# Kernel optimization log

Hardware: AMD Instinct MI355X
Metric: run time of the kernel (lower is better)

The kernel has to match this reference:

```python
import math
import jax, jax.numpy as jnp
import numpy as np

LAMDA = 0.5
ALPHA = 0.1
N_NODES = 100000
N_EDGES = 1600000
NFEAT = 512
NHID = 128
NCLASS = 40
NLAYER = 4


def setup_inputs() -> dict:
    key = jax.random.key(0)
    ks = jax.random.split(key, 9)
    x = jax.random.normal(ks[0], (N_NODES, NFEAT), dtype=jnp.float32)
    rows = jnp.sort(jax.random.randint(ks[1], (N_EDGES,), 0, N_NODES, dtype=jnp.int32))
    cols = jax.random.randint(ks[2], (N_EDGES,), 0, N_NODES, dtype=jnp.int32)
    # positive edge weights (stand-in for symmetric-normalized adjacency values)
    vals = jax.random.uniform(ks[3], (N_EDGES,), dtype=jnp.float32) * 0.1
    stdv_hid = 1.0 / math.sqrt(NHID)
    fc1_w = jax.random.normal(ks[4], (NFEAT, NHID), dtype=jnp.float32) * 0.02
    fc1_b = jnp.zeros((NHID,), dtype=jnp.float32)
    conv_w = jax.random.uniform(ks[5], (NLAYER, NHID, NHID), dtype=jnp.float32,
                                minval=-stdv_hid, maxval=stdv_hid)
    fc2_w = jax.random.normal(ks[6], (NHID, NCLASS), dtype=jnp.float32) * 0.02
    fc2_b = jnp.zeros((NCLASS,), dtype=jnp.float32)
    return {"x": x, "rows": rows, "cols": cols, "vals": vals,
            "fc1_w": fc1_w, "fc1_b": fc1_b, "conv_w": conv_w,
            "fc2_w": fc2_w, "fc2_b": fc2_b}


def reference(x, rows, cols, vals, fc1_w, fc1_b, conv_w, fc2_w, fc2_b):
    n = x.shape[0]
    # input projection + relu (dropout is identity in eval mode)
    h = jax.nn.relu(x @ fc1_w + fc1_b)  # [N, nhid]
    h0 = h
    for i in range(conv_w.shape[0]):
        theta = math.log(LAMDA / (i + 1) + 1.0)
        # sparse spmm: hi = A @ h  via gather + segment-sum scatter
        hi = jax.ops.segment_sum(vals[:, None] * h[cols], rows, num_segments=n)
        support = (1.0 - ALPHA) * hi + ALPHA * h0  # initial-residual mix
        h = jax.nn.relu(theta * (support @ conv_w[i]) + (1.0 - theta) * support)
    logits = h @ fc2_w + fc2_b  # [N, nclass]
    return (jax.nn.log_softmax(logits, axis=1), h, jnp.concatenate([h, logits], axis=1))
```

## Files before the change

### kernel.cpp

```cpp
#include <hip/hip_runtime.h>
#include <math.h>

#define N_NODES 100000
#define NFEAT 512
#define NHID 128
#define NCLASS 40

typedef unsigned int uint;
typedef unsigned short ushort;
typedef unsigned char uchar;
typedef short bf16x8 __attribute__((ext_vector_type(8)));
typedef float f32x4 __attribute__((ext_vector_type(4)));
typedef float f32x2 __attribute__((ext_vector_type(2)));

__device__ inline ushort bf16s(float a) {
    uint u = __float_as_uint(a);
    return (ushort)((u + 0x7fffu + ((u >> 16) & 1u)) >> 16);
}
__device__ inline uint bf16pack(float a, float b) {
    return (uint)bf16s(a) | ((uint)bf16s(b) << 16);
}
__device__ inline float bf16tof(ushort u) { return __uint_as_float(((uint)u) << 16); }
__device__ inline float bflo(uint u) { return __uint_as_float(u << 16); }
__device__ inline float bfhi(uint u) { return __uint_as_float(u & 0xffff0000u); }

__device__ inline uchar fp8byte(float v) {
    uint pk = __builtin_amdgcn_cvt_pk_fp8_f32(v, 0.f, 0u, false);
    return (uchar)(pk & 0xffu);
}

__global__ void prep_weights(const float* __restrict__ fc1_w, const float* __restrict__ conv_w,
                             ushort* __restrict__ wT1, ushort* __restrict__ wTc) {
    int idx = blockIdx.x * 256 + threadIdx.x;
    {   int n = idx >> 9, k = idx & 511;
        wT1[idx] = bf16s(fc1_w[k * NHID + n]); }
    {   int L = idx >> 14, rem = idx & 16383;
        int n = rem >> 7, k = rem & 127;
        wTc[idx] = bf16s(conv_w[L * 16384 + k * NHID + n]); }
}

__global__ void rowptr_kernel(const int* __restrict__ rows, int* __restrict__ rowptr, int nE) {
    int i = blockIdx.x * blockDim.x + threadIdx.x;
    if (i > N_NODES) return;
    int lo = 0, hi = nE;
    while (lo < hi) { int mid = (lo + hi) >> 1; if (rows[mid] < i) lo = mid + 1; else hi = mid; }
    rowptr[i] = lo;
}

__global__ void __launch_bounds__(256) fc1_mfma(const float* __restrict__ x,
                                                const uint* __restrict__ wT1,
                                                const float* __restrict__ bias,
                                                ushort* __restrict__ h0b,
                                                uchar* __restrict__ hf8) {
    __shared__ ushort As[32][72];
    __shared__ ushort Bs[128][72];
    const int tid = threadIdx.x;
    const int lane = tid & 63;
    const int wave = tid >> 6;
    const int wr = wave >> 1, wc = wave & 1;
    const int r0 = blockIdx.x * 32;

    f32x4 acc[4] = {};

    for (int ks = 0; ks < NFEAT; ks += 64) {
        {   int row = tid >> 3, kq = tid & 7;
            const float* xp = x + (size_t)(r0 + row) * NFEAT + ks + kq * 8;
            float4 v0 = *reinterpret_cast<const float4*>(xp);
            float4 v1 = *reinterpret_cast<const float4*>(xp + 4);
            uint4 pk;
            pk.x = bf16pack(v0.x, v0.y); pk.y = bf16pack(v0.z, v0.w);
            pk.z = bf16pack(v1.x, v1.y); pk.w = bf16pack(v1.z, v1.w);
            *reinterpret_cast<uint4*>(&As[row][kq * 8]) = pk;
        }
        #pragma unroll
        for (int p = 0; p < 4; ++p) {
            int idx = tid + p * 256;
            int n = idx >> 3, q = idx & 7;
            uint4 w4 = *reinterpret_cast<const uint4*>(wT1 + n * 256 + (ks >> 1) + q * 4);
            *reinterpret_cast<uint4*>(&Bs[n][q * 8]) = w4;
        }
        __syncthreads();
        #pragma unroll
        for (int ks2 = 0; ks2 < 64; ks2 += 32) {
            bf16x8 a = *reinterpret_cast<const bf16x8*>(&As[wr * 16 + (lane & 15)][ks2 + (lane >> 4) * 8]);
            #pragma unroll
            for (int j = 0; j < 4; ++j) {
                bf16x8 b = *reinterpret_cast<const bf16x8*>(&Bs[wc * 64 + j * 16 + (lane & 15)][ks2 + (lane >> 4) * 8]);
                acc[j] = __builtin_amdgcn_mfma_f32_16x16x32_bf16(a, b, acc[j], 0, 0, 0);
            }
        }
        __syncthreads();
    }

    const int cb = wc * 64 + (lane & 15);
    const int rb = r0 + wr * 16 + ((lane >> 4) << 2);
    #pragma unroll
    for (int j = 0; j < 4; ++j) {
        int col = cb + j * 16;
        float bj = bias[col];
        #pragma unroll
        for (int i = 0; i < 4; ++i) {
            float v = fmaxf(acc[j][i] + bj, 0.f);
            h0b[(size_t)(rb + i) * NHID + col] = bf16s(v);
            hf8[(size_t)(rb + i) * NHID + col] = fp8byte(v);
        }
    }
}

__global__ void __launch_bounds__(256) spmm_kernel(
        const uint2* __restrict__ h8,
        const uint4* __restrict__ h0b4,
        const int* __restrict__ rowptr,
        const int* __restrict__ cols,
        const float* __restrict__ vals,
        uint4* __restrict__ sb4) {
    const int node = blockIdx.x * 4 + (threadIdx.x >> 6);
    const int lane = threadIdx.x & 63;
    const int q = lane >> 4;
    const int l = lane & 15;

    const int e0 = rowptr[node], e1 = rowptr[node + 1];

    f32x2 a0 = {0.f, 0.f}, a1 = {0.f, 0.f}, a2 = {0.f, 0.f}, a3 = {0.f, 0.f};
    #pragma unroll 4
    for (int e = e0 + q; e < e1; e += 4) {
        int   c = cols[e];
        float v = vals[e];
        uint2 hv = h8[(size_t)c * 16 + l];
        f32x2 p0 = __builtin_amdgcn_cvt_pk_f32_fp8(hv.x, false);
        f32x2 p1 = __builtin_amdgcn_cvt_pk_f32_fp8(hv.x, true);
        f32x2 p2 = __builtin_amdgcn_cvt_pk_f32_fp8(hv.y, false);
        f32x2 p3 = __builtin_amdgcn_cvt_pk_f32_fp8(hv.y, true);
        f32x2 vv = {v, v};
        a0 += vv * p0;
        a1 += vv * p1;
        a2 += vv * p2;
        a3 += vv * p3;
    }

    #pragma unroll
    for (int d = 16; d <= 32; d <<= 1) {
        a0.x += __shfl_xor(a0.x, d); a0.y += __shfl_xor(a0.y, d);
        a1.x += __shfl_xor(a1.x, d); a1.y += __shfl_xor(a1.y, d);
        a2.x += __shfl_xor(a2.x, d); a2.y += __shfl_xor(a2.y, d);
        a3.x += __shfl_xor(a3.x, d); a3.y += __shfl_xor(a3.y, d);
    }

    if (q == 0) {
        uint4 h0v = h0b4[(size_t)node * 16 + l];
        uint4 o;
        o.x = bf16pack(0.9f * a0.x + 0.1f * bflo(h0v.x), 0.9f * a0.y + 0.1f * bfhi(h0v.x));
        o.y = bf16pack(0.9f * a1.x + 0.1f * bflo(h0v.y), 0.9f * a1.y + 0.1f * bfhi(h0v.y));
        o.z = bf16pack(0.9f * a2.x + 0.1f * bflo(h0v.z), 0.9f * a2.y + 0.1f * bfhi(h0v.z));
        o.w = bf16pack(0.9f * a3.x + 0.1f * bflo(h0v.w), 0.9f * a3.y + 0.1f * bfhi(h0v.w));
        sb4[(size_t)node * 16 + l] = o;
    }
}

__global__ void __launch_bounds__(256) layer_mfma(const uint* __restrict__ sb,
                                                  const uint* __restrict__ wTc,
                                                  float theta,
                                                  uchar* __restrict__ hf8,
                                                  float* __restrict__ fout) {
    __shared__ ushort As[64][136];
    __shared__ ushort Bs[128][136];
    const int tid = threadIdx.x;
    const int lane = tid & 63;
    const int wave = tid >> 6;
    const int wr = wave >> 1, wc = wave & 1;
    const int r0 = blockIdx.x * 64;

    #pragma unroll
    for (int p = 0; p < 4; ++p) {
        int idx = tid + p * 256;
        int row = idx >> 4, kq = idx & 15;
        uint4 v = *reinterpret_cast<const uint4*>(sb + (size_t)(r0 + row) * 64 + kq * 4);
        *reinterpret_cast<uint4*>(&As[row][kq * 8]) = v;
    }
    #pragma unroll
    for (int p = 0; p < 8; ++p) {
        int idx = tid + p * 256;
        int n = idx >> 4, kq = idx & 15;
        uint4 v = *reinterpret_cast<const uint4*>(wTc + n * 64 + kq * 4);
        *reinterpret_cast<uint4*>(&Bs[n][kq * 8]) = v;
    }
    __syncthreads();

    f32x4 acc[2][4] = {};
    #pragma unroll
    for (int ks = 0; ks < NHID; ks += 32) {
        #pragma unroll
        for (int mr = 0; mr < 2; ++mr) {
            bf16x8 a = *reinterpret_cast<const bf16x8*>(&As[wr * 32 + mr * 16 + (lane & 15)][ks + (lane >> 4) * 8]);
            #pragma unroll
            for (int j = 0; j < 4; ++j) {
                bf16x8 b = *reinterpret_cast<const bf16x8*>(&Bs[wc * 64 + j * 16 + (lane & 15)][ks + (lane >> 4) * 8]);
                acc[mr][j] = __builtin_amdgcn_mfma_f32_16x16x32_bf16(a, b, acc[mr][j], 0, 0, 0);
            }
        }
    }

    const float om = 1.f - theta;
    #pragma unroll
    for (int mr = 0; mr < 2; ++mr) {
        const int rloc = wr * 32 + mr * 16 + ((lane >> 4) << 2);
        #pragma unroll
        for (int j = 0; j < 4; ++j) {
            int col = wc * 64 + j * 16 + (lane & 15);
            #pragma unroll
            for (int i = 0; i < 4; ++i) {
                int gr = r0 + rloc + i;
                if (gr < N_NODES) {
                    float s = bf16tof(As[rloc + i][col]);
                    float v = fmaxf(fmaf(theta, acc[mr][j][i], om * s), 0.f);
                    if (fout) fout[(size_t)gr * NHID + col] = v;
                    else      hf8[(size_t)gr * NHID + col] = fp8byte(v);
                }
            }
        }
    }
}

__global__ void final_kernel(const float* __restrict__ h, const float* __restrict__ w,
                             const float* __restrict__ b, float* __restrict__ out0,
                             float* __restrict__ out2) {
    __shared__ float hs[4][128];
    const int s = threadIdx.x >> 6;
    const int lane = threadIdx.x & 63;
    const int node = blockIdx.x * 4 + s;

    float h_lo = h[node * NHID + lane];
    float h_hi = h[node * NHID + 64 + lane];
    hs[s][lane] = h_lo;
    hs[s][64 + lane] = h_hi;
    __syncthreads();

    float logit = 0.f;
    if (lane < NCLASS) {
        logit = b[lane];
        #pragma unroll 8
        for (int k = 0; k < NHID; ++k)
            logit = fmaf(hs[s][k], w[k * NCLASS + lane], logit);
    }

    float mv = (lane < NCLASS) ? logit : -1e30f;
    #pragma unroll
    for (int m = 32; m; m >>= 1) mv = fmaxf(mv, __shfl_xor(mv, m));
    float ev = (lane < NCLASS) ? __expf(logit - mv) : 0.f;
    float sum = ev;
    #pragma unroll
    for (int m = 32; m; m >>= 1) sum += __shfl_xor(sum, m);
    float lse = mv + __logf(sum);

    if (lane < NCLASS) {
        out0[node * NCLASS + lane] = logit - lse;
        out2[node * 168 + 128 + lane] = logit;
    }
    out2[node * 168 + lane] = h_lo;
    out2[node * 168 + 64 + lane] = h_hi;
}

extern "C" void kernel_launch(void* const* d_in, const int* in_sizes, int n_in,
                              void* d_out, int out_size, void* d_ws, size_t ws_size,
                              hipStream_t stream) {
    const float* x      = (const float*)d_in[0];
    const int*   rows   = (const int*)  d_in[1];
    const int*   cols   = (const int*)  d_in[2];
    const float* vals   = (const float*)d_in[3];
    const float* fc1_w  = (const float*)d_in[4];
    const float* fc1_b  = (const float*)d_in[5];
    const float* conv_w = (const float*)d_in[6];
    const float* fc2_w  = (const float*)d_in[7];
    const float* fc2_b  = (const float*)d_in[8];
    float* out = (float*)d_out;

    const int nE = in_sizes[1];
    const size_t NH = (size_t)N_NODES * NHID;
    const size_t PAD = 64 * NHID;

    char* p = (char*)d_ws;
    int*    rowptr = (int*)p;          p += 400128;
    ushort* h0b    = (ushort*)p;       p += NH * 2;
    ushort* sb     = (ushort*)p;       p += (NH + PAD) * 2;
    uchar*  hf8    = (uchar*)p;        p += NH;
    ushort* wT1    = (ushort*)p;       p += 65536 * 2;
    ushort* wTc    = (ushort*)p;       p += 65536 * 2;

    float* out0 = out;
    float* out1 = out + (size_t)N_NODES * NCLASS;
    float* out2 = out1 + NH;

    prep_weights<<<256, 256, 0, stream>>>(fc1_w, conv_w, wT1, wTc);
    rowptr_kernel<<<(N_NODES + 1 + 255) / 256, 256, 0, stream>>>(rows, rowptr, nE);
    fc1_mfma<<<N_NODES / 32, 256, 0, stream>>>(x, (const uint*)wT1, fc1_b, h0b, hf8);

    for (int i = 0; i < 4; ++i) {
        float theta = logf(0.5f / (float)(i + 1) + 1.0f);
        spmm_kernel<<<N_NODES / 4, 256, 0, stream>>>(
            (const uint2*)hf8, (const uint4*)h0b, rowptr, cols, vals, (uint4*)sb);
        layer_mfma<<<(N_NODES + 63) / 64, 256, 0, stream>>>(
            (const uint*)sb, (const uint*)(wTc + (size_t)i * 16384), theta,
            hf8, (i == 3) ? out1 : nullptr);
    }

    final_kernel<<<N_NODES / 4, 256, 0, stream>>>(out1, fc2_w, fc2_b, out0, out2);
}
```

Before: 463.5 us.

## Interleave edge metadata, widen SpMM gathers to 16B, enlarge fc1 row tile

Adds a pre-pass that packs each edge's column index and weight into one 8-byte record, so the SpMM loop issues a single nontemporal load per edge instead of two. The SpMM now processes 8 edges per step, with each group of 8 lanes gathering 16 bytes of the fp8 neighbour row, and reduces across three shuffle levels instead of two. The fc1 GEMM tile grows from 32 to 64 rows per block, with clamped loads and a guarded store for the tail, which halves the number of weight-tile reloads per row. The cost is an extra preprocessing kernel, 8 bytes per edge of extra workspace, and more accumulator registers in both kernels.

```diff
diff --git a/kernel.cpp b/kernel.cpp
--- a/kernel.cpp
+++ b/kernel.cpp
@@ -39,6 +39,15 @@
         wTc[idx] = bf16s(conv_w[L * 16384 + k * NHID + n]); }
 }
 
+__global__ void prep_meta(const int* __restrict__ cols, const float* __restrict__ vals,
+                          int2* __restrict__ emeta, int nE) {
+    int e = blockIdx.x * 256 + threadIdx.x;
+    if (e < nE) {
+        int2 m; m.x = cols[e]; m.y = __float_as_int(vals[e]);
+        emeta[e] = m;
+    }
+}
+
 __global__ void rowptr_kernel(const int* __restrict__ rows, int* __restrict__ rowptr, int nE) {
     int i = blockIdx.x * blockDim.x + threadIdx.x;
     if (i > N_NODES) return;
@@ -52,25 +61,32 @@
                                                 const float* __restrict__ bias,
                                                 ushort* __restrict__ h0b,
                                                 uchar* __restrict__ hf8) {
-    __shared__ ushort As[32][72];
+    __shared__ ushort As[64][72];
     __shared__ ushort Bs[128][72];
     const int tid = threadIdx.x;
     const int lane = tid & 63;
     const int wave = tid >> 6;
     const int wr = wave >> 1, wc = wave & 1;
-    const int r0 = blockIdx.x * 32;
-
-    f32x4 acc[4] = {};
+    const int r0 = blockIdx.x * 64;
+
+    f32x4 acc[2][4] = {};
 
     for (int ks = 0; ks < NFEAT; ks += 64) {
-        {   int row = tid >> 3, kq = tid & 7;
-            const float* xp = x + (size_t)(r0 + row) * NFEAT + ks + kq * 8;
+        {
+            int row = tid >> 2, kq = tid & 3;
+            int gr = r0 + row; if (gr > N_NODES - 1) gr = N_NODES - 1;
+            const float* xp = x + (size_t)gr * NFEAT + ks + kq * 16;
             float4 v0 = *reinterpret_cast<const float4*>(xp);
             float4 v1 = *reinterpret_cast<const float4*>(xp + 4);
-            uint4 pk;
-            pk.x = bf16pack(v0.x, v0.y); pk.y = bf16pack(v0.z, v0.w);
-            pk.z = bf16pack(v1.x, v1.y); pk.w = bf16pack(v1.z, v1.w);
-            *reinterpret_cast<uint4*>(&As[row][kq * 8]) = pk;
+            float4 v2 = *reinterpret_cast<const float4*>(xp + 8);
+            float4 v3 = *reinterpret_cast<const float4*>(xp + 12);
+            uint4 p0, p1;
+            p0.x = bf16pack(v0.x, v0.y); p0.y = bf16pack(v0.z, v0.w);
+            p0.z = bf16pack(v1.x, v1.y); p0.w = bf16pack(v1.z, v1.w);
+            p1.x = bf16pack(v2.x, v2.y); p1.y = bf16pack(v2.z, v2.w);
+            p1.z = bf16pack(v3.x, v3.y); p1.w = bf16pack(v3.z, v3.w);
+            *reinterpret_cast<uint4*>(&As[row][kq * 16]) = p0;
+            *reinterpret_cast<uint4*>(&As[row][kq * 16 + 8]) = p1;
         }
         #pragma unroll
         for (int p = 0; p < 4; ++p) {
@@ -82,78 +98,99 @@
         __syncthreads();
         #pragma unroll
         for (int ks2 = 0; ks2 < 64; ks2 += 32) {
-            bf16x8 a = *reinterpret_cast<const bf16x8*>(&As[wr * 16 + (lane & 15)][ks2 + (lane >> 4) * 8]);
             #pragma unroll
-            for (int j = 0; j < 4; ++j) {
-                bf16x8 b = *reinterpret_cast<const bf16x8*>(&Bs[wc * 64 + j * 16 + (lane & 15)][ks2 + (lane >> 4) * 8]);
-                acc[j] = __builtin_amdgcn_mfma_f32_16x16x32_bf16(a, b, acc[j], 0, 0, 0);
+            for (int mr = 0; mr < 2; ++mr) {
+                bf16x8 a = *reinterpret_cast<const bf16x8*>(
+                    &As[wr * 32 + mr * 16 + (lane & 15)][ks2 + (lane >> 4) * 8]);
+                #pragma unroll
+                for (int j = 0; j < 4; ++j) {
+                    bf16x8 b = *reinterpret_cast<const bf16x8*>(
+                        &Bs[wc * 64 + j * 16 + (lane & 15)][ks2 + (lane >> 4) * 8]);
+                    acc[mr][j] = __builtin_amdgcn_mfma_f32_16x16x32_bf16(a, b, acc[mr][j], 0, 0, 0);
+                }
             }
         }
         __syncthreads();
     }
 
     const int cb = wc * 64 + (lane & 15);
-    const int rb = r0 + wr * 16 + ((lane >> 4) << 2);
-    #pragma unroll
-    for (int j = 0; j < 4; ++j) {
-        int col = cb + j * 16;
-        float bj = bias[col];
-        #pragma unroll
-        for (int i = 0; i < 4; ++i) {
-            float v = fmaxf(acc[j][i] + bj, 0.f);
-            h0b[(size_t)(rb + i) * NHID + col] = bf16s(v);
-            hf8[(size_t)(rb + i) * NHID + col] = fp8byte(v);
+    #pragma unroll
+    for (int mr = 0; mr < 2; ++mr) {
+        const int rloc = wr * 32 + mr * 16 + ((lane >> 4) << 2);
+        #pragma unroll
+        for (int j = 0; j < 4; ++j) {
+            int col = cb + j * 16;
+            float bj = bias[col];
+            #pragma unroll
+            for (int i = 0; i < 4; ++i) {
+                int gr = r0 + rloc + i;
+                if (gr < N_NODES) {
+                    float v = fmaxf(acc[mr][j][i] + bj, 0.f);
+                    h0b[(size_t)gr * NHID + col] = bf16s(v);
+                    hf8[(size_t)gr * NHID + col] = fp8byte(v);
+                }
+            }
         }
     }
 }
 
 __global__ void __launch_bounds__(256) spmm_kernel(
-        const uint2* __restrict__ h8,
+        const uint4* __restrict__ h8,
         const uint4* __restrict__ h0b4,
         const int* __restrict__ rowptr,
-        const int* __restrict__ cols,
-        const float* __restrict__ vals,
+        const long long* __restrict__ emeta,
         uint4* __restrict__ sb4) {
     const int node = blockIdx.x * 4 + (threadIdx.x >> 6);
     const int lane = threadIdx.x & 63;
-    const int q = lane >> 4;
-    const int l = lane & 15;
+    const int oct = lane >> 3;
+    const int l = lane & 7;
 
     const int e0 = rowptr[node], e1 = rowptr[node + 1];
 
-    f32x2 a0 = {0.f, 0.f}, a1 = {0.f, 0.f}, a2 = {0.f, 0.f}, a3 = {0.f, 0.f};
-    #pragma unroll 4
-    for (int e = e0 + q; e < e1; e += 4) {
-        int   c = cols[e];
-        float v = vals[e];
-        uint2 hv = h8[(size_t)c * 16 + l];
-        f32x2 p0 = __builtin_amdgcn_cvt_pk_f32_fp8(hv.x, false);
-        f32x2 p1 = __builtin_amdgcn_cvt_pk_f32_fp8(hv.x, true);
-        f32x2 p2 = __builtin_amdgcn_cvt_pk_f32_fp8(hv.y, false);
-        f32x2 p3 = __builtin_amdgcn_cvt_pk_f32_fp8(hv.y, true);
+    f32x2 acc[8] = {};
+
+    #pragma unroll 2
+    for (int base = e0; base < e1; base += 8) {
+        const int m = e1 - base;
+        int ee = (oct < m) ? (base + oct) : base;
+        long long md = __builtin_nontemporal_load(emeta + ee);
+        float v = (oct < m) ? __int_as_float((int)(md >> 32)) : 0.f;
+        int   c = (int)md;
+        uint4 hv = h8[(size_t)c * 8 + l];
         f32x2 vv = {v, v};
-        a0 += vv * p0;
-        a1 += vv * p1;
-        a2 += vv * p2;
-        a3 += vv * p3;
-    }
-
-    #pragma unroll
-    for (int d = 16; d <= 32; d <<= 1) {
-        a0.x += __shfl_xor(a0.x, d); a0.y += __shfl_xor(a0.y, d);
-        a1.x += __shfl_xor(a1.x, d); a1.y += __shfl_xor(a1.y, d);
-        a2.x += __shfl_xor(a2.x, d); a2.y += __shfl_xor(a2.y, d);
-        a3.x += __shfl_xor(a3.x, d); a3.y += __shfl_xor(a3.y, d);
-    }
-
-    if (q == 0) {
-        uint4 h0v = h0b4[(size_t)node * 16 + l];
-        uint4 o;
-        o.x = bf16pack(0.9f * a0.x + 0.1f * bflo(h0v.x), 0.9f * a0.y + 0.1f * bfhi(h0v.x));
-        o.y = bf16pack(0.9f * a1.x + 0.1f * bflo(h0v.y), 0.9f * a1.y + 0.1f * bfhi(h0v.y));
-        o.z = bf16pack(0.9f * a2.x + 0.1f * bflo(h0v.z), 0.9f * a2.y + 0.1f * bfhi(h0v.z));
-        o.w = bf16pack(0.9f * a3.x + 0.1f * bflo(h0v.w), 0.9f * a3.y + 0.1f * bfhi(h0v.w));
-        sb4[(size_t)node * 16 + l] = o;
+        acc[0] += vv * __builtin_amdgcn_cvt_pk_f32_fp8(hv.x, false);
+        acc[1] += vv * __builtin_amdgcn_cvt_pk_f32_fp8(hv.x, true);
+        acc[2] += vv * __builtin_amdgcn_cvt_pk_f32_fp8(hv.y, false);
+        acc[3] += vv * __builtin_amdgcn_cvt_pk_f32_fp8(hv.y, true);
+        acc[4] += vv * __builtin_amdgcn_cvt_pk_f32_fp8(hv.z, false);
+        acc[5] += vv * __builtin_amdgcn_cvt_pk_f32_fp8(hv.z, true);
+        acc[6] += vv * __builtin_amdgcn_cvt_pk_f32_fp8(hv.w, false);
+        acc[7] += vv * __builtin_amdgcn_cvt_pk_f32_fp8(hv.w, true);
+    }
+
+    #pragma unroll
+    for (int d = 8; d <= 32; d <<= 1) {
+        #pragma unroll
+        for (int k = 0; k < 8; ++k) {
+            acc[k].x += __shfl_xor(acc[k].x, d);
+            acc[k].y += __shfl_xor(acc[k].y, d);
+        }
+    }
+
+    if (oct == 0) {
+        uint4 h0a = h0b4[(size_t)node * 16 + 2 * l];
+        uint4 h0bv = h0b4[(size_t)node * 16 + 2 * l + 1];
+        uint4 oa, ob;
+        oa.x = bf16pack(0.9f * acc[0].x + 0.1f * bflo(h0a.x), 0.9f * acc[0].y + 0.1f * bfhi(h0a.x));
+        oa.y = bf16pack(0.9f * acc[1].x + 0.1f * bflo(h0a.y), 0.9f * acc[1].y + 0.1f * bfhi(h0a.y));
+        oa.z = bf16pack(0.9f * acc[2].x + 0.1f * bflo(h0a.z), 0.9f * acc[2].y + 0.1f * bfhi(h0a.z));
+        oa.w = bf16pack(0.9f * acc[3].x + 0.1f * bflo(h0a.w), 0.9f * acc[3].y + 0.1f * bfhi(h0a.w));
+        ob.x = bf16pack(0.9f * acc[4].x + 0.1f * bflo(h0bv.x), 0.9f * acc[4].y + 0.1f * bfhi(h0bv.x));
+        ob.y = bf16pack(0.9f * acc[5].x + 0.1f * bflo(h0bv.y), 0.9f * acc[5].y + 0.1f * bfhi(h0bv.y));
+        ob.z = bf16pack(0.9f * acc[6].x + 0.1f * bflo(h0bv.z), 0.9f * acc[6].y + 0.1f * bfhi(h0bv.z));
+        ob.w = bf16pack(0.9f * acc[7].x + 0.1f * bflo(h0bv.w), 0.9f * acc[7].y + 0.1f * bfhi(h0bv.w));
+        sb4[(size_t)node * 16 + 2 * l]     = oa;
+        sb4[(size_t)node * 16 + 2 * l + 1] = ob;
     }
 }
 
@@ -283,6 +320,7 @@
     ushort* h0b    = (ushort*)p;       p += NH * 2;
     ushort* sb     = (ushort*)p;       p += (NH + PAD) * 2;
     uchar*  hf8    = (uchar*)p;        p += NH;
+    int2*   emeta  = (int2*)p;         p += (size_t)nE * 8;
     ushort* wT1    = (ushort*)p;       p += 65536 * 2;
     ushort* wTc    = (ushort*)p;       p += 65536 * 2;
 
@@ -291,13 +329,14 @@
     float* out2 = out1 + NH;
 
     prep_weights<<<256, 256, 0, stream>>>(fc1_w, conv_w, wT1, wTc);
+    prep_meta<<<(nE + 255) / 256, 256, 0, stream>>>(cols, vals, emeta, nE);
     rowptr_kernel<<<(N_NODES + 1 + 255) / 256, 256, 0, stream>>>(rows, rowptr, nE);
-    fc1_mfma<<<N_NODES / 32, 256, 0, stream>>>(x, (const uint*)wT1, fc1_b, h0b, hf8);
+    fc1_mfma<<<(N_NODES + 63) / 64, 256, 0, stream>>>(x, (const uint*)wT1, fc1_b, h0b, hf8);
 
     for (int i = 0; i < 4; ++i) {
         float theta = logf(0.5f / (float)(i + 1) + 1.0f);
         spmm_kernel<<<N_NODES / 4, 256, 0, stream>>>(
-            (const uint2*)hf8, (const uint4*)h0b, rowptr, cols, vals, (uint4*)sb);
+            (const uint4*)hf8, (const uint4*)h0b, rowptr, (const long long*)emeta, (uint4*)sb);
         layer_mfma<<<(N_NODES + 63) / 64, 256, 0, stream>>>(
             (const uint*)sb, (const uint*)(wTc + (size_t)i * 16384), theta,
             hf8, (i == 3) ? out1 : nullptr);
```

Result: slower. 493.6 us (+6.5%).

## Enlarge fc1 row tile to 64 and split layer weight staging into K halves

Applied to the files above, without the earlier changes.

The fc1 GEMM now processes 64 rows per block instead of 32. Each wave computes two 16-row MFMA tiles, so every staged weight tile is reused across twice as many rows and fc1_w is reloaded fewer times; the last partial block is handled by clamping input rows and guarding stores. The layer GEMM now stages the weight matrix in two K-halves with a smaller LDS buffer, which cuts shared memory per block and may allow more blocks per CU. The cost is an extra pair of barriers and a second weight load in the middle of the layer kernel.

```diff
diff --git a/kernel.cpp b/kernel.cpp
--- a/kernel.cpp
+++ b/kernel.cpp
@@ -52,25 +52,32 @@
                                                 const float* __restrict__ bias,
                                                 ushort* __restrict__ h0b,
                                                 uchar* __restrict__ hf8) {
-    __shared__ ushort As[32][72];
+    __shared__ ushort As[64][72];
     __shared__ ushort Bs[128][72];
     const int tid = threadIdx.x;
     const int lane = tid & 63;
     const int wave = tid >> 6;
     const int wr = wave >> 1, wc = wave & 1;
-    const int r0 = blockIdx.x * 32;
-
-    f32x4 acc[4] = {};
+    const int r0 = blockIdx.x * 64;
+
+    f32x4 acc[2][4] = {};
 
     for (int ks = 0; ks < NFEAT; ks += 64) {
-        {   int row = tid >> 3, kq = tid & 7;
-            const float* xp = x + (size_t)(r0 + row) * NFEAT + ks + kq * 8;
+        {
+            int row = tid >> 2, kq = tid & 3;
+            int gr = r0 + row; if (gr > N_NODES - 1) gr = N_NODES - 1;
+            const float* xp = x + (size_t)gr * NFEAT + ks + kq * 16;
             float4 v0 = *reinterpret_cast<const float4*>(xp);
             float4 v1 = *reinterpret_cast<const float4*>(xp + 4);
-            uint4 pk;
-            pk.x = bf16pack(v0.x, v0.y); pk.y = bf16pack(v0.z, v0.w);
-            pk.z = bf16pack(v1.x, v1.y); pk.w = bf16pack(v1.z, v1.w);
-            *reinterpret_cast<uint4*>(&As[row][kq * 8]) = pk;
+            float4 v2 = *reinterpret_cast<const float4*>(xp + 8);
+            float4 v3 = *reinterpret_cast<const float4*>(xp + 12);
+            uint4 p0, p1;
+            p0.x = bf16pack(v0.x, v0.y); p0.y = bf16pack(v0.z, v0.w);
+            p0.z = bf16pack(v1.x, v1.y); p0.w = bf16pack(v1.z, v1.w);
+            p1.x = bf16pack(v2.x, v2.y); p1.y = bf16pack(v2.z, v2.w);
+            p1.z = bf16pack(v3.x, v3.y); p1.w = bf16pack(v3.z, v3.w);
+            *reinterpret_cast<uint4*>(&As[row][kq * 16]) = p0;
+            *reinterpret_cast<uint4*>(&As[row][kq * 16 + 8]) = p1;
         }
         #pragma unroll
         for (int p = 0; p < 4; ++p) {
@@ -82,27 +89,38 @@
         __syncthreads();
         #pragma unroll
         for (int ks2 = 0; ks2 < 64; ks2 += 32) {
-            bf16x8 a = *reinterpret_cast<const bf16x8*>(&As[wr * 16 + (lane & 15)][ks2 + (lane >> 4) * 8]);
-            #pragma unroll
-            for (int j = 0; j < 4; ++j) {
-                bf16x8 b = *reinterpret_cast<const bf16x8*>(&Bs[wc * 64 + j * 16 + (lane & 15)][ks2 + (lane >> 4) * 8]);
-                acc[j] = __builtin_amdgcn_mfma_f32_16x16x32_bf16(a, b, acc[j], 0, 0, 0);
+            #pragma unroll
+            for (int mr = 0; mr < 2; ++mr) {
+                bf16x8 a = *reinterpret_cast<const bf16x8*>(
+                    &As[wr * 32 + mr * 16 + (lane & 15)][ks2 + (lane >> 4) * 8]);
+                #pragma unroll
+                for (int j = 0; j < 4; ++j) {
+                    bf16x8 b = *reinterpret_cast<const bf16x8*>(
+                        &Bs[wc * 64 + j * 16 + (lane & 15)][ks2 + (lane >> 4) * 8]);
+                    acc[mr][j] = __builtin_amdgcn_mfma_f32_16x16x32_bf16(a, b, acc[mr][j], 0, 0, 0);
+                }
             }
         }
         __syncthreads();
     }
 
     const int cb = wc * 64 + (lane & 15);
-    const int rb = r0 + wr * 16 + ((lane >> 4) << 2);
-    #pragma unroll
-    for (int j = 0; j < 4; ++j) {
-        int col = cb + j * 16;
-        float bj = bias[col];
-        #pragma unroll
-        for (int i = 0; i < 4; ++i) {
-            float v = fmaxf(acc[j][i] + bj, 0.f);
-            h0b[(size_t)(rb + i) * NHID + col] = bf16s(v);
-            hf8[(size_t)(rb + i) * NHID + col] = fp8byte(v);
+    #pragma unroll
+    for (int mr = 0; mr < 2; ++mr) {
+        const int rloc = wr * 32 + mr * 16 + ((lane >> 4) << 2);
+        #pragma unroll
+        for (int j = 0; j < 4; ++j) {
+            int col = cb + j * 16;
+            float bj = bias[col];
+            #pragma unroll
+            for (int i = 0; i < 4; ++i) {
+                int gr = r0 + rloc + i;
+                if (gr < N_NODES) {
+                    float v = fmaxf(acc[mr][j][i] + bj, 0.f);
+                    h0b[(size_t)gr * NHID + col] = bf16s(v);
+                    hf8[(size_t)gr * NHID + col] = fp8byte(v);
+                }
+            }
         }
     }
 }
@@ -163,7 +181,7 @@
                                                   uchar* __restrict__ hf8,
                                                   float* __restrict__ fout) {
     __shared__ ushort As[64][136];
-    __shared__ ushort Bs[128][136];
+    __shared__ ushort Bs[128][72];
     const int tid = threadIdx.x;
     const int lane = tid & 63;
     const int wave = tid >> 6;
@@ -173,29 +191,45 @@
     #pragma unroll
     for (int p = 0; p < 4; ++p) {
         int idx = tid + p * 256;
+        int n = idx >> 3, q = idx & 7;
+        uint4 v = *reinterpret_cast<const uint4*>(wTc + n * 64 + q * 4);
+        *reinterpret_cast<uint4*>(&Bs[n][q * 8]) = v;
+    }
+    #pragma unroll
+    for (int p = 0; p < 4; ++p) {
+        int idx = tid + p * 256;
         int row = idx >> 4, kq = idx & 15;
         uint4 v = *reinterpret_cast<const uint4*>(sb + (size_t)(r0 + row) * 64 + kq * 4);
         *reinterpret_cast<uint4*>(&As[row][kq * 8]) = v;
     }
-    #pragma unroll
-    for (int p = 0; p < 8; ++p) {
-        int idx = tid + p * 256;
-        int n = idx >> 4, kq = idx & 15;
-        uint4 v = *reinterpret_cast<const uint4*>(wTc + n * 64 + kq * 4);
-        *reinterpret_cast<uint4*>(&Bs[n][kq * 8]) = v;
-    }
     __syncthreads();
 
     f32x4 acc[2][4] = {};
     #pragma unroll
-    for (int ks = 0; ks < NHID; ks += 32) {
-        #pragma unroll
-        for (int mr = 0; mr < 2; ++mr) {
-            bf16x8 a = *reinterpret_cast<const bf16x8*>(&As[wr * 32 + mr * 16 + (lane & 15)][ks + (lane >> 4) * 8]);
-            #pragma unroll
-            for (int j = 0; j < 4; ++j) {
-                bf16x8 b = *reinterpret_cast<const bf16x8*>(&Bs[wc * 64 + j * 16 + (lane & 15)][ks + (lane >> 4) * 8]);
-                acc[mr][j] = __builtin_amdgcn_mfma_f32_16x16x32_bf16(a, b, acc[mr][j], 0, 0, 0);
+    for (int halfk = 0; halfk < 2; ++halfk) {
+        if (halfk) {
+            __syncthreads();
+            #pragma unroll
+            for (int p = 0; p < 4; ++p) {
+                int idx = tid + p * 256;
+                int n = idx >> 3, q = idx & 7;
+                uint4 v = *reinterpret_cast<const uint4*>(wTc + n * 64 + 32 + q * 4);
+                *reinterpret_cast<uint4*>(&Bs[n][q * 8]) = v;
+            }
+            __syncthreads();
+        }
+        #pragma unroll
+        for (int ks2 = 0; ks2 < 64; ks2 += 32) {
+            #pragma unroll
+            for (int mr = 0; mr < 2; ++mr) {
+                bf16x8 a = *reinterpret_cast<const bf16x8*>(
+                    &As[wr * 32 + mr * 16 + (lane & 15)][halfk * 64 + ks2 + (lane >> 4) * 8]);
+                #pragma unroll
+                for (int j = 0; j < 4; ++j) {
+                    bf16x8 b = *reinterpret_cast<const bf16x8*>(
+                        &Bs[wc * 64 + j * 16 + (lane & 15)][ks2 + (lane >> 4) * 8]);
+                    acc[mr][j] = __builtin_amdgcn_mfma_f32_16x16x32_bf16(a, b, acc[mr][j], 0, 0, 0);
+                }
             }
         }
     }
@@ -292,7 +326,7 @@
 
     prep_weights<<<256, 256, 0, stream>>>(fc1_w, conv_w, wT1, wTc);
     rowptr_kernel<<<(N_NODES + 1 + 255) / 256, 256, 0, stream>>>(rows, rowptr, nE);
-    fc1_mfma<<<N_NODES / 32, 256, 0, stream>>>(x, (const uint*)wT1, fc1_b, h0b, hf8);
+    fc1_mfma<<<(N_NODES + 63) / 64, 256, 0, stream>>>(x, (const uint*)wT1, fc1_b, h0b, hf8);
 
     for (int i = 0; i < 4; ++i) {
         float theta = logf(0.5f / (float)(i + 1) + 1.0f);
```

Measured after the change: 464.1 us. About the same (+0.1%).
